# Optimization experiments

Measured on AMD Instinct MI355X. Metric: run time of the kernel, lower is better.

Reference implementation:

```python
import jax, jax.numpy as jnp
import numpy as np

B, N, D, H, E, K = 8, 4096, 128, 256, 16, 2


def setup_inputs() -> dict:
    key = jax.random.key(0)
    ks = jax.random.split(key, 11)
    sc = 0.05
    return {
        "x":   jax.random.normal(ks[0], (B, N, D), jnp.float32),
        "Wg":  jax.random.normal(ks[1], (D, E), jnp.float32) * sc,
        "bg":  jnp.zeros((E,), jnp.float32),
        "W1":  jax.random.normal(ks[2], (E, D, H), jnp.float32) * sc,
        "b1":  jnp.zeros((E, H), jnp.float32),
        "W2":  jax.random.normal(ks[3], (E, H, D), jnp.float32) * sc,
        "b2":  jnp.zeros((E, D), jnp.float32),
        "Wu1": jax.random.normal(ks[4], (D, H), jnp.float32) * sc,
        "bu1": jnp.zeros((H,), jnp.float32),
        "Wu2": jax.random.normal(ks[5], (H, D), jnp.float32) * sc,
        "bu2": jnp.zeros((D,), jnp.float32),
    }


def reference(x, Wg, bg, W1, b1, W2, b2, Wu1, bu1, Wu2, bu2):
    b, n, d = x.shape
    xt = x.reshape(b * n, d)                       # [T, D]
    T = xt.shape[0]

    # gating: top-k logits kept, rest -inf, then softmax -> zeros off top-k
    logits = xt @ Wg + bg                          # [T, E]
    topv, topi = jax.lax.top_k(logits, K)          # [T, K]
    mask = jnp.full_like(logits, -jnp.inf)
    mask = mask.at[jnp.arange(T)[:, None], topi].set(topv)
    gate = jax.nn.softmax(mask, axis=-1)           # [T, E]

    # dense all-expert MLP (matches original torch.stack over experts)
    h = jax.nn.relu(jnp.einsum('td,edh->teh', xt, W1) + b1)   # [T, E, H]
    eo = jnp.einsum('teh,ehd->ted', h, W2) + b2               # [T, E, D]

    # universal expert scaled by omega = 1 - max gate
    omega = 1.0 - jnp.max(gate, axis=1, keepdims=True)        # [T, 1]
    uni = omega * (jax.nn.relu(xt @ Wu1 + bu1) @ Wu2 + bu2)   # [T, D]

    out = jnp.einsum('te,ted->td', gate, eo) + uni
    return out.reshape(b, n, d)
```

## Files before the change

kernel.cpp:

```cpp
#include <hip/hip_runtime.h>
#include <hip/hip_bf16.h>

constexpr int kT = 32768;
constexpr int kD = 128;
constexpr int kH = 256;
constexpr int kE = 16;

typedef __bf16 bf16x8 __attribute__((ext_vector_type(8)));
typedef unsigned short u16x8 __attribute__((ext_vector_type(8)));
typedef float f32x4 __attribute__((ext_vector_type(4)));

#define LDX 136

constexpr int NB_TP   = 272;
constexpr int NB_GATE = kT / 64;
constexpr int CNT_STRIDE = 32;
constexpr int MOE_GRID = 1552;

__device__ __forceinline__ unsigned short f2bf(float f) {
  unsigned int u = __float_as_uint(f);
  u += 0x7FFFu + ((u >> 16) & 1u);
  return (unsigned short)(u >> 16);
}
__device__ __forceinline__ float bf2f(unsigned short s) {
  return __uint_as_float((unsigned int)s << 16);
}

__global__ __launch_bounds__(256) void front_kernel(
    const float* __restrict__ x, const float* __restrict__ Wg,
    const float* __restrict__ bg,
    const float* __restrict__ W1, const float* __restrict__ W2,
    const float* __restrict__ Wu1, const float* __restrict__ Wu2,
    unsigned short* __restrict__ xb, unsigned short* __restrict__ W1t,
    unsigned short* __restrict__ W2t, unsigned short* __restrict__ Wu1t,
    unsigned short* __restrict__ Wu2t,
    int* __restrict__ cnt, int* __restrict__ btok, float* __restrict__ bgate,
    int* __restrict__ tpos)
{
  __shared__ __align__(16) char smem[46848];
  const int tid = threadIdx.x;
  const int b = blockIdx.x;

  if (b < NB_TP) {
    int bb = b;
    const float* src; unsigned short* dst; int R, C, r0, c0;
    if (bb < 136) {
      int m = bb >> 3, t8 = bb & 7;
      R = 128; C = 256;
      src = (m < 16) ? W1 + (size_t)m * 32768 : Wu1;
      dst = (m < 16) ? W1t + (size_t)m * 32768 : Wu1t;
      r0 = (t8 & 1) * 64; c0 = (t8 >> 1) * 64;
    } else {
      bb -= 136;
      int m = bb >> 3, t8 = bb & 7;
      R = 256; C = 128;
      src = (m < 16) ? W2 + (size_t)m * 32768 : Wu2;
      dst = (m < 16) ? W2t + (size_t)m * 32768 : Wu2t;
      r0 = (t8 >> 1) * 64; c0 = (t8 & 1) * 64;
    }
    unsigned short (*tl)[72] = reinterpret_cast<unsigned short(*)[72]>(smem);
#pragma unroll
    for (int i = 0; i < 4; ++i) {
      int s = i * 256 + tid;
      int r = s >> 4, c4 = s & 15;
      float4 v = *reinterpret_cast<const float4*>(&src[(size_t)(r0 + r) * C + c0 + c4 * 4]);
      tl[c4 * 4 + 0][r] = f2bf(v.x);
      tl[c4 * 4 + 1][r] = f2bf(v.y);
      tl[c4 * 4 + 2][r] = f2bf(v.z);
      tl[c4 * 4 + 3][r] = f2bf(v.w);
    }
    __syncthreads();
#pragma unroll
    for (int i = 0; i < 2; ++i) {
      int s = i * 256 + tid;
      int c = s >> 3, seg = s & 7;
      uint4 v = *reinterpret_cast<const uint4*>(&tl[c][seg * 8]);
      *reinterpret_cast<uint4*>(&dst[(size_t)(c0 + c) * R + r0 + seg * 8]) = v;
    }
    return;
  }

  {
    float* sWt = reinterpret_cast<float*>(smem);
    float* sX  = reinterpret_cast<float*>(smem + 8448);
    float* sL  = reinterpret_cast<float*>(smem + 42240);
    int* hcnt  = reinterpret_cast<int*>(smem + 46592);
    int* hbase = reinterpret_cast<int*>(smem + 46656);
    int* hb16  = reinterpret_cast<int*>(smem + 46720);
    const int t0 = (b - NB_TP) * 64;

    if (tid < kE) hcnt[tid] = 0;
    for (int i = tid; i < kD * kE; i += 256) {
      int d = i >> 4, e = i & 15;
      sWt[e * 132 + d] = Wg[i];
    }
    const float4* xv = reinterpret_cast<const float4*>(x + (size_t)t0 * kD);
    for (int i = tid; i < 64 * kD / 4; i += 256) {
      int r = i >> 5, c4 = i & 31;
      *reinterpret_cast<float4*>(&sX[r * 132 + c4 * 4]) = xv[i];
    }
    __syncthreads();

    const int e = tid & 15, tq = tid >> 4;
    const double bgd = (double)bg[e];
    const float4* wr = reinterpret_cast<const float4*>(&sWt[e * 132]);
#pragma unroll
    for (int p = 0; p < 4; ++p) {
      int tt = p * 16 + tq;
      const float4* xr = reinterpret_cast<const float4*>(&sX[tt * 132]);
      double a0 = 0.0, a1 = 0.0, a2 = 0.0, a3 = 0.0;
#pragma unroll
      for (int d8 = 0; d8 < 8; ++d8) {
        float4 xa0 = xr[d8 * 4 + 0], wa0 = wr[d8 * 4 + 0];
        float4 xa1 = xr[d8 * 4 + 1], wa1 = wr[d8 * 4 + 1];
        float4 xa2 = xr[d8 * 4 + 2], wa2 = wr[d8 * 4 + 2];
        float4 xa3 = xr[d8 * 4 + 3], wa3 = wr[d8 * 4 + 3];
        a0 += (double)xa0.x * (double)wa0.x + (double)xa0.y * (double)wa0.y
            + (double)xa0.z * (double)wa0.z + (double)xa0.w * (double)wa0.w;
        a1 += (double)xa1.x * (double)wa1.x + (double)xa1.y * (double)wa1.y
            + (double)xa1.z * (double)wa1.z + (double)xa1.w * (double)wa1.w;
        a2 += (double)xa2.x * (double)wa2.x + (double)xa2.y * (double)wa2.y
            + (double)xa2.z * (double)wa2.z + (double)xa2.w * (double)wa2.w;
        a3 += (double)xa3.x * (double)wa3.x + (double)xa3.y * (double)wa3.y
            + (double)xa3.z * (double)wa3.z + (double)xa3.w * (double)wa3.w;
      }
      sL[tt * 17 + e] = (float)(((a0 + a1) + (a2 + a3)) + bgd);
    }
#pragma unroll
    for (int p = 0; p < 4; ++p) {
      int idx = p * 256 + tid;
      int r = idx >> 4, c8 = (idx & 15) * 8;
      const float* sp = &sX[r * 132 + c8];
      u16x8 v;
#pragma unroll
      for (int j = 0; j < 8; ++j) v[j] = f2bf(sp[j]);
      *reinterpret_cast<u16x8*>(&xb[(size_t)(t0 + r) * kD + c8]) = v;
    }
    __syncthreads();

    int e0 = 0, e1 = 0, lp0 = 0, lp1 = 0;
    float g0 = 0.f, g1 = 0.f;
    const int t = t0 + tid;
    if (tid < 64) {
      float v0 = -3.4e38f, v1 = -3.4e38f;
      for (int i = 0; i < kE; ++i) {
        float v = sL[tid * 17 + i];
        if (v > v0) { v1 = v0; e1 = e0; v0 = v; e0 = i; }
        else if (v > v1) { v1 = v; e1 = i; }
      }
      float r = expf(v1 - v0);
      g0 = 1.f / (1.f + r);
      g1 = 1.f - g0;
      lp0 = atomicAdd(&hcnt[e0], 1);
      lp1 = atomicAdd(&hcnt[e1], 1);
    }
    if (tid == 0) hb16[0] = atomicAdd(&cnt[16 * CNT_STRIDE], 64);
    __syncthreads();
    if (tid < kE)
      hbase[tid] = atomicAdd(&cnt[tid * CNT_STRIDE], hcnt[tid]);
    __syncthreads();
    if (tid < 64) {
      int p0 = hbase[e0] + lp0;
      btok[e0 * kT + p0] = t; bgate[e0 * kT + p0] = g0;
      int p1 = hbase[e1] + lp1;
      btok[e1 * kT + p1] = t; bgate[e1 * kT + p1] = g1;
      int p2 = hb16[0] + tid;
      btok[16 * kT + p2] = t; bgate[16 * kT + p2] = 1.f - g0;
      tpos[2 * t]     = (e0 << 16) | p0;
      tpos[2 * t + 1] = (e1 << 16) | p1;
    }
  }
}

__global__ __launch_bounds__(256) void moe_kernel(
    const unsigned short* __restrict__ xb,
    const unsigned short* __restrict__ W1t,
    const unsigned short* __restrict__ W2t,
    const unsigned short* __restrict__ Wu1t,
    const unsigned short* __restrict__ Wu2t,
    const float* __restrict__ b1, const float* __restrict__ b2,
    const float* __restrict__ bu1, const float* __restrict__ bu2,
    const int* __restrict__ cnt, const int* __restrict__ btok,
    const float* __restrict__ bgate,
    unsigned short* __restrict__ eo, float* __restrict__ out)
{
  __shared__ alignas(16) char smem[35328];
  unsigned short* xs = reinterpret_cast<unsigned short*>(smem);
  unsigned short* hs = reinterpret_cast<unsigned short*>(smem + 17408);
  int*   toks = reinterpret_cast<int*>(smem + 34816);
  float* gts  = reinterpret_cast<float*>(smem + 35072);
  unsigned short* stB = reinterpret_cast<unsigned short*>(smem);
  float* stF = reinterpret_cast<float*>(smem);
  const int tid = threadIdx.x;
  const int bid = blockIdx.x;

  int c17[17];
#pragma unroll
  for (int i = 0; i < 17; ++i) c17[i] = cnt[i * CNT_STRIDE];
  int e = -1, tile = 0, eobase = 0, accb = 0;
#pragma unroll
  for (int i = 0; i < 17; ++i) {
    int tl = (c17[i] + 63) >> 6;
    if (e < 0) {
      if (bid < accb + tl) { e = i; tile = bid - accb; }
      else { accb += tl; if (i < 16) eobase += c17[i]; }
    }
  }
  if (e < 0) return;
  const int rows = min(64, c17[e] - tile * 64);

  const int w = tid >> 6, l = tid & 63, lr = l & 15, lg = l >> 4;
  const int gr = tid >> 4, gc = (tid & 15) * 8;
  const f32x4 z4 = {0.f, 0.f, 0.f, 0.f};

  const unsigned short* Bw1 = (e < 16) ? W1t + (size_t)e * kH * kD : Wu1t;
  const unsigned short* Bw2 = (e < 16) ? W2t + (size_t)e * kD * kH : Wu2t;
  const float* bs1 = (e < 16) ? b1 + (size_t)e * kH : bu1;
  const float* bs2 = (e < 16) ? b2 + (size_t)e * kD : bu2;

  {
    int tokR[4]; float gtR[4];
#pragma unroll
    for (int p = 0; p < 4; ++p) {
      int r = p * 16 + gr; bool v = r < rows; int bi2 = e * kT + tile * 64 + r;
      tokR[p] = v ? btok[bi2] : 0;
      gtR[p]  = v ? bgate[bi2] : 0.f;
    }
#pragma unroll
    for (int p = 0; p < 4; ++p) {
      uint4 v = *reinterpret_cast<const uint4*>(xb + (size_t)tokR[p] * kD + gc);
      *reinterpret_cast<uint4*>(&xs[(p * 16 + gr) * LDX + gc]) = v;
    }
    if ((tid & 15) == 0) {
#pragma unroll
      for (int p = 0; p < 4; ++p) {
        toks[p * 16 + gr] = tokR[p];
        gts[p * 16 + gr]  = gtR[p];
      }
    }
  }
  float b2v[2];
#pragma unroll
  for (int n = 0; n < 2; ++n) b2v[n] = bs2[w * 32 + n * 16 + lr];
  f32x4 acc2[4][2];
#pragma unroll
  for (int m = 0; m < 4; ++m)
#pragma unroll
    for (int n = 0; n < 2; ++n) acc2[m][n] = z4;
  __syncthreads();

#pragma unroll
  for (int hf = 0; hf < 2; ++hf) {
    bf16x8 Bf[2][4];
#pragma unroll
    for (int n = 0; n < 2; ++n)
#pragma unroll
      for (int kk = 0; kk < 4; ++kk)
        Bf[n][kk] = *reinterpret_cast<const bf16x8*>(
            Bw1 + (size_t)(hf * 128 + w * 32 + n * 16 + lr) * kD + kk * 32 + lg * 8);
    float b1v[2];
#pragma unroll
    for (int n = 0; n < 2; ++n) b1v[n] = bs1[hf * 128 + w * 32 + n * 16 + lr];
    f32x4 acc[4][2];
#pragma unroll
    for (int m = 0; m < 4; ++m)
#pragma unroll
      for (int n = 0; n < 2; ++n) acc[m][n] = z4;
#pragma unroll
    for (int kk = 0; kk < 4; ++kk) {
      bf16x8 a[4];
#pragma unroll
      for (int m = 0; m < 4; ++m)
        a[m] = *reinterpret_cast<const bf16x8*>(xs + (m * 16 + lr) * LDX + kk * 32 + lg * 8);
#pragma unroll
      for (int m = 0; m < 4; ++m)
#pragma unroll
        for (int n = 0; n < 2; ++n)
          acc[m][n] = __builtin_amdgcn_mfma_f32_16x16x32_bf16(a[m], Bf[n][kk], acc[m][n], 0, 0, 0);
    }
#pragma unroll
    for (int n = 0; n < 2; ++n) {
      const int hc = w * 32 + n * 16 + lr;
      const float bs = b1v[n];
#pragma unroll
      for (int m = 0; m < 4; ++m)
#pragma unroll
        for (int q = 0; q < 4; ++q) {
          float v = acc[m][n][q] + bs;
          v = fmaxf(v, 0.f);
          hs[(m * 16 + lg * 4 + q) * LDX + hc] = f2bf(v);
        }
    }
    __syncthreads();

    bf16x8 B2f[2][4];
#pragma unroll
    for (int n = 0; n < 2; ++n)
#pragma unroll
      for (int kk = 0; kk < 4; ++kk)
        B2f[n][kk] = *reinterpret_cast<const bf16x8*>(
            Bw2 + (size_t)(w * 32 + n * 16 + lr) * kH + hf * 128 + kk * 32 + lg * 8);
#pragma unroll
    for (int kk = 0; kk < 4; ++kk) {
      bf16x8 a[4];
#pragma unroll
      for (int m = 0; m < 4; ++m)
        a[m] = *reinterpret_cast<const bf16x8*>(hs + (m * 16 + lr) * LDX + kk * 32 + lg * 8);
#pragma unroll
      for (int m = 0; m < 4; ++m)
#pragma unroll
        for (int n = 0; n < 2; ++n)
          acc2[m][n] = __builtin_amdgcn_mfma_f32_16x16x32_bf16(a[m], B2f[n][kk], acc2[m][n], 0, 0, 0);
    }
    __syncthreads();
  }

  if (e < 16) {
#pragma unroll
    for (int m = 0; m < 4; ++m)
#pragma unroll
      for (int q = 0; q < 4; ++q) {
        int r = m * 16 + lg * 4 + q;
        float g = gts[r];
#pragma unroll
        for (int n = 0; n < 2; ++n)
          stB[r * LDX + w * 32 + n * 16 + lr] = f2bf(g * (acc2[m][n][q] + b2v[n]));
      }
    __syncthreads();
    unsigned short* dst = eo + (size_t)(eobase + tile * 64) * kD;
#pragma unroll
    for (int j = 0; j < 4; ++j) {
      int gidx = j * 256 + tid;
      int r = gidx >> 4, seg = gidx & 15;
      if (r < rows) {
        uint4 v = *reinterpret_cast<const uint4*>(&stB[r * LDX + seg * 8]);
        *reinterpret_cast<uint4*>(dst + (size_t)r * kD + seg * 8) = v;
      }
    }
  } else {
#pragma unroll
    for (int m = 0; m < 4; ++m)
#pragma unroll
      for (int q = 0; q < 4; ++q) {
        int r = m * 16 + lg * 4 + q;
        float g = gts[r];
#pragma unroll
        for (int n = 0; n < 2; ++n)
          stF[r * 132 + w * 32 + n * 16 + lr] = g * (acc2[m][n][q] + b2v[n]);
      }
    __syncthreads();
#pragma unroll
    for (int j = 0; j < 8; ++j) {
      int gidx = j * 1024 + tid * 4;
      int r = gidx >> 7, cc = gidx & 127;
      if (r < rows) {
        int tok = toks[r];
        float4 v = *reinterpret_cast<const float4*>(&stF[r * 132 + cc]);
        *reinterpret_cast<float4*>(out + (size_t)tok * kD + cc) = v;
      }
    }
  }
}

__global__ __launch_bounds__(256) void combine_kernel(
    const int* __restrict__ cnt, const int* __restrict__ tpos,
    const unsigned short* __restrict__ eo, float* __restrict__ out)
{
  __shared__ int base[16];
  const int tid = threadIdx.x;
  if (tid < 16) {
    int s = 0;
    for (int i = 0; i < tid; ++i) s += cnt[i * CNT_STRIDE];
    base[tid] = s;
  }
  __syncthreads();
  const int tk = blockIdx.x * 16 + (tid >> 4);
  const int c = tid & 15;
  int a0 = tpos[2 * tk], a1 = tpos[2 * tk + 1];
  size_t r0 = (size_t)(base[a0 >> 16] + (a0 & 0xffff)) * kD + c * 8;
  size_t r1 = (size_t)(base[a1 >> 16] + (a1 & 0xffff)) * kD + c * 8;
  u16x8 v0 = *reinterpret_cast<const u16x8*>(eo + r0);
  u16x8 v1 = *reinterpret_cast<const u16x8*>(eo + r1);
  float s[8];
#pragma unroll
  for (int j = 0; j < 8; ++j) s[j] = bf2f(v0[j]) + bf2f(v1[j]);
  float4* op = reinterpret_cast<float4*>(out + (size_t)tk * kD + c * 8);
  float4 o0 = op[0], o1 = op[1];
  o0.x += s[0]; o0.y += s[1]; o0.z += s[2]; o0.w += s[3];
  o1.x += s[4]; o1.y += s[5]; o1.z += s[6]; o1.w += s[7];
  op[0] = o0; op[1] = o1;
}

extern "C" void kernel_launch(void* const* d_in, const int* in_sizes, int n_in,
                              void* d_out, int out_size, void* d_ws, size_t ws_size,
                              hipStream_t stream) {
  (void)in_sizes; (void)n_in; (void)out_size; (void)ws_size;
  const float* x   = (const float*)d_in[0];
  const float* Wg  = (const float*)d_in[1];
  const float* bg  = (const float*)d_in[2];
  const float* W1  = (const float*)d_in[3];
  const float* b1  = (const float*)d_in[4];
  const float* W2  = (const float*)d_in[5];
  const float* b2  = (const float*)d_in[6];
  const float* Wu1 = (const float*)d_in[7];
  const float* bu1 = (const float*)d_in[8];
  const float* Wu2 = (const float*)d_in[9];
  const float* bu2 = (const float*)d_in[10];
  float* out = (float*)d_out;

  char* ws = (char*)d_ws;
  constexpr size_t OFF_XB    = 0;
  constexpr size_t OFF_W1T   = 8388608;
  constexpr size_t OFF_W2T   = 9437184;
  constexpr size_t OFF_WU1T  = 10485760;
  constexpr size_t OFF_WU2T  = 10551296;
  constexpr size_t OFF_CNT   = 10616832;
  constexpr size_t OFF_TPOS  = 10620928;
  constexpr size_t OFF_BTOK  = 10883072;
  constexpr size_t OFF_BGATE = 13111296;
  constexpr size_t OFF_EO    = 15339520;

  unsigned short* xb   = (unsigned short*)(ws + OFF_XB);
  unsigned short* W1t  = (unsigned short*)(ws + OFF_W1T);
  unsigned short* W2t  = (unsigned short*)(ws + OFF_W2T);
  unsigned short* Wu1t = (unsigned short*)(ws + OFF_WU1T);
  unsigned short* Wu2t = (unsigned short*)(ws + OFF_WU2T);
  int*   cnt   = (int*)(ws + OFF_CNT);
  int*   tpos  = (int*)(ws + OFF_TPOS);
  int*   btok  = (int*)(ws + OFF_BTOK);
  float* bgate = (float*)(ws + OFF_BGATE);
  unsigned short* eo = (unsigned short*)(ws + OFF_EO);

  hipMemsetAsync(cnt, 0, 17 * CNT_STRIDE * sizeof(int), stream);
  front_kernel<<<NB_TP + NB_GATE, 256, 0, stream>>>(
      x, Wg, bg, W1, W2, Wu1, Wu2,
      xb, W1t, W2t, Wu1t, Wu2t, cnt, btok, bgate, tpos);
  moe_kernel<<<MOE_GRID, 256, 0, stream>>>(
      xb, W1t, W2t, Wu1t, Wu2t, b1, b2, bu1, bu2, cnt, btok, bgate, eo, out);
  combine_kernel<<<kT / 16, 256, 0, stream>>>(cnt, tpos, eo, out);
}
```

Before: 81.91 us.

## Shrink MoE shared memory by chunking hidden dim into quarters and staging output in halves

Result: no change. 81.90 us (-0.0%).

```diff
diff --git a/kernel.cpp b/kernel.cpp
--- a/kernel.cpp
+++ b/kernel.cpp
@@ -11,6 +11,7 @@
 typedef float f32x4 __attribute__((ext_vector_type(4)));
 
 #define LDX 136
+#define LDQ 72
 
 constexpr int NB_TP   = 272;
 constexpr int NB_GATE = kT / 64;
@@ -104,28 +105,20 @@
     const int e = tid & 15, tq = tid >> 4;
     const double bgd = (double)bg[e];
     const float4* wr = reinterpret_cast<const float4*>(&sWt[e * 132]);
-#pragma unroll
-    for (int p = 0; p < 4; ++p) {
-      int tt = p * 16 + tq;
-      const float4* xr = reinterpret_cast<const float4*>(&sX[tt * 132]);
-      double a0 = 0.0, a1 = 0.0, a2 = 0.0, a3 = 0.0;
-#pragma unroll
-      for (int d8 = 0; d8 < 8; ++d8) {
-        float4 xa0 = xr[d8 * 4 + 0], wa0 = wr[d8 * 4 + 0];
-        float4 xa1 = xr[d8 * 4 + 1], wa1 = wr[d8 * 4 + 1];
-        float4 xa2 = xr[d8 * 4 + 2], wa2 = wr[d8 * 4 + 2];
-        float4 xa3 = xr[d8 * 4 + 3], wa3 = wr[d8 * 4 + 3];
-        a0 += (double)xa0.x * (double)wa0.x + (double)xa0.y * (double)wa0.y
-            + (double)xa0.z * (double)wa0.z + (double)xa0.w * (double)wa0.w;
-        a1 += (double)xa1.x * (double)wa1.x + (double)xa1.y * (double)wa1.y
-            + (double)xa1.z * (double)wa1.z + (double)xa1.w * (double)wa1.w;
-        a2 += (double)xa2.x * (double)wa2.x + (double)xa2.y * (double)wa2.y
-            + (double)xa2.z * (double)wa2.z + (double)xa2.w * (double)wa2.w;
-        a3 += (double)xa3.x * (double)wa3.x + (double)xa3.y * (double)wa3.y
-            + (double)xa3.z * (double)wa3.z + (double)xa3.w * (double)wa3.w;
-      }
-      sL[tt * 17 + e] = (float)(((a0 + a1) + (a2 + a3)) + bgd);
-    }
+    double acc[4] = {0.0, 0.0, 0.0, 0.0};
+#pragma unroll
+    for (int d4 = 0; d4 < 32; ++d4) {
+      float4 wa = wr[d4];
+#pragma unroll
+      for (int p = 0; p < 4; ++p) {
+        float4 xa = *reinterpret_cast<const float4*>(&sX[(p * 16 + tq) * 132 + d4 * 4]);
+        acc[p] += (double)xa.x * (double)wa.x + (double)xa.y * (double)wa.y
+                + (double)xa.z * (double)wa.z + (double)xa.w * (double)wa.w;
+      }
+    }
+#pragma unroll
+    for (int p = 0; p < 4; ++p)
+      sL[(p * 16 + tq) * 17 + e] = (float)(acc[p] + bgd);
 #pragma unroll
     for (int p = 0; p < 4; ++p) {
       int idx = p * 256 + tid;
@@ -184,11 +177,11 @@
     const float* __restrict__ bgate,
     unsigned short* __restrict__ eo, float* __restrict__ out)
 {
-  __shared__ alignas(16) char smem[35328];
+  __shared__ alignas(16) char smem[27136];
   unsigned short* xs = reinterpret_cast<unsigned short*>(smem);
   unsigned short* hs = reinterpret_cast<unsigned short*>(smem + 17408);
-  int*   toks = reinterpret_cast<int*>(smem + 34816);
-  float* gts  = reinterpret_cast<float*>(smem + 35072);
+  int*   toks = reinterpret_cast<int*>(smem + 26624);
+  float* gts  = reinterpret_cast<float*>(smem + 26880);
   unsigned short* stB = reinterpret_cast<unsigned short*>(smem);
   float* stF = reinterpret_cast<float*>(smem);
   const int tid = threadIdx.x;
@@ -250,22 +243,17 @@
   __syncthreads();
 
 #pragma unroll
-  for (int hf = 0; hf < 2; ++hf) {
-    bf16x8 Bf[2][4];
-#pragma unroll
-    for (int n = 0; n < 2; ++n)
-#pragma unroll
-      for (int kk = 0; kk < 4; ++kk)
-        Bf[n][kk] = *reinterpret_cast<const bf16x8*>(
-            Bw1 + (size_t)(hf * 128 + w * 32 + n * 16 + lr) * kD + kk * 32 + lg * 8);
-    float b1v[2];
-#pragma unroll
-    for (int n = 0; n < 2; ++n) b1v[n] = bs1[hf * 128 + w * 32 + n * 16 + lr];
-    f32x4 acc[4][2];
-#pragma unroll
-    for (int m = 0; m < 4; ++m)
-#pragma unroll
-      for (int n = 0; n < 2; ++n) acc[m][n] = z4;
+  for (int hq = 0; hq < 4; ++hq) {
+    const int hcol = hq * 64 + w * 16 + lr;
+    bf16x8 Bf[4];
+#pragma unroll
+    for (int kk = 0; kk < 4; ++kk)
+      Bf[kk] = *reinterpret_cast<const bf16x8*>(
+          Bw1 + (size_t)hcol * kD + kk * 32 + lg * 8);
+    const float b1q = bs1[hcol];
+    f32x4 acc[4];
+#pragma unroll
+    for (int m = 0; m < 4; ++m) acc[m] = z4;
 #pragma unroll
     for (int kk = 0; kk < 4; ++kk) {
       bf16x8 a[4];
@@ -274,43 +262,36 @@
         a[m] = *reinterpret_cast<const bf16x8*>(xs + (m * 16 + lr) * LDX + kk * 32 + lg * 8);
 #pragma unroll
       for (int m = 0; m < 4; ++m)
+        acc[m] = __builtin_amdgcn_mfma_f32_16x16x32_bf16(a[m], Bf[kk], acc[m], 0, 0, 0);
+    }
+#pragma unroll
+    for (int m = 0; m < 4; ++m)
+#pragma unroll
+      for (int q = 0; q < 4; ++q) {
+        float v = acc[m][q] + b1q;
+        v = fmaxf(v, 0.f);
+        hs[(m * 16 + lg * 4 + q) * LDQ + w * 16 + lr] = f2bf(v);
+      }
+    __syncthreads();
+
+    bf16x8 B2f[2][2];
+#pragma unroll
+    for (int n = 0; n < 2; ++n)
+#pragma unroll
+      for (int k2 = 0; k2 < 2; ++k2)
+        B2f[n][k2] = *reinterpret_cast<const bf16x8*>(
+            Bw2 + (size_t)(w * 32 + n * 16 + lr) * kH + hq * 64 + k2 * 32 + lg * 8);
+#pragma unroll
+    for (int k2 = 0; k2 < 2; ++k2) {
+      bf16x8 a[4];
+#pragma unroll
+      for (int m = 0; m < 4; ++m)
+        a[m] = *reinterpret_cast<const bf16x8*>(hs + (m * 16 + lr) * LDQ + k2 * 32 + lg * 8);
+#pragma unroll
+      for (int m = 0; m < 4; ++m)
 #pragma unroll
         for (int n = 0; n < 2; ++n)
-          acc[m][n] = __builtin_amdgcn_mfma_f32_16x16x32_bf16(a[m], Bf[n][kk], acc[m][n], 0, 0, 0);
-    }
-#pragma unroll
-    for (int n = 0; n < 2; ++n) {
-      const int hc = w * 32 + n * 16 + lr;
-      const float bs = b1v[n];
-#pragma unroll
-      for (int m = 0; m < 4; ++m)
-#pragma unroll
-        for (int q = 0; q < 4; ++q) {
-          float v = acc[m][n][q] + bs;
-          v = fmaxf(v, 0.f);
-          hs[(m * 16 + lg * 4 + q) * LDX + hc] = f2bf(v);
-        }
-    }
-    __syncthreads();
-
-    bf16x8 B2f[2][4];
-#pragma unroll
-    for (int n = 0; n < 2; ++n)
-#pragma unroll
-      for (int kk = 0; kk < 4; ++kk)
-        B2f[n][kk] = *reinterpret_cast<const bf16x8*>(
-            Bw2 + (size_t)(w * 32 + n * 16 + lr) * kH + hf * 128 + kk * 32 + lg * 8);
-#pragma unroll
-    for (int kk = 0; kk < 4; ++kk) {
-      bf16x8 a[4];
-#pragma unroll
-      for (int m = 0; m < 4; ++m)
-        a[m] = *reinterpret_cast<const bf16x8*>(hs + (m * 16 + lr) * LDX + kk * 32 + lg * 8);
-#pragma unroll
-      for (int m = 0; m < 4; ++m)
-#pragma unroll
-        for (int n = 0; n < 2; ++n)
-          acc2[m][n] = __builtin_amdgcn_mfma_f32_16x16x32_bf16(a[m], B2f[n][kk], acc2[m][n], 0, 0, 0);
+          acc2[m][n] = __builtin_amdgcn_mfma_f32_16x16x32_bf16(a[m], B2f[n][k2], acc2[m][n], 0, 0, 0);
     }
     __syncthreads();
   }
@@ -339,25 +320,31 @@
     }
   } else {
 #pragma unroll
-    for (int m = 0; m < 4; ++m)
-#pragma unroll
-      for (int q = 0; q < 4; ++q) {
-        int r = m * 16 + lg * 4 + q;
-        float g = gts[r];
-#pragma unroll
-        for (int n = 0; n < 2; ++n)
-          stF[r * 132 + w * 32 + n * 16 + lr] = g * (acc2[m][n][q] + b2v[n]);
-      }
-    __syncthreads();
-#pragma unroll
-    for (int j = 0; j < 8; ++j) {
-      int gidx = j * 1024 + tid * 4;
-      int r = gidx >> 7, cc = gidx & 127;
-      if (r < rows) {
-        int tok = toks[r];
-        float4 v = *reinterpret_cast<const float4*>(&stF[r * 132 + cc]);
-        *reinterpret_cast<float4*>(out + (size_t)tok * kD + cc) = v;
-      }
+    for (int ch = 0; ch < 2; ++ch) {
+      if ((w >> 1) == ch) {
+#pragma unroll
+        for (int m = 0; m < 4; ++m)
+#pragma unroll
+          for (int q = 0; q < 4; ++q) {
+            int r = m * 16 + lg * 4 + q;
+            float g = gts[r];
+#pragma unroll
+            for (int n = 0; n < 2; ++n)
+              stF[r * 68 + (w & 1) * 32 + n * 16 + lr] = g * (acc2[m][n][q] + b2v[n]);
+          }
+      }
+      __syncthreads();
+#pragma unroll
+      for (int j = 0; j < 4; ++j) {
+        int gidx = j * 256 + tid;
+        int r = gidx >> 4, seg = gidx & 15;
+        if (r < rows) {
+          int tok = toks[r];
+          float4 v = *reinterpret_cast<const float4*>(&stF[r * 68 + seg * 4]);
+          *reinterpret_cast<float4*>(out + (size_t)tok * kD + ch * 64 + seg * 4) = v;
+        }
+      }
+      __syncthreads();
     }
   }
 }
```
